# Performance work log

Measured on AMD Instinct MI355X. Metric: run time of the kernel, lower is better.

## Reference

```python
import jax, jax.numpy as jnp
import numpy as np

B, T, N, F = 16, 24, 2048, 64


def setup_inputs() -> dict:
    key = jax.random.key(0)
    kx, k1, k2, k3, kb, kv = jax.random.split(key, 6)
    x = jax.random.normal(kx, (B, T, N, F), dtype=jnp.float32)
    # xavier_uniform for U2 (N,F) and Ve (T,T); uniform(0,1) for U1, U3, be
    lim_u2 = float(np.sqrt(6.0 / (N + F)))
    lim_ve = float(np.sqrt(6.0 / (T + T)))
    U1 = jax.random.uniform(k1, (N,), dtype=jnp.float32)
    U2 = jax.random.uniform(k2, (N, F), dtype=jnp.float32, minval=-lim_u2, maxval=lim_u2)
    U3 = jax.random.uniform(k3, (F,), dtype=jnp.float32)
    be = jax.random.uniform(kb, (T, T), dtype=jnp.float32)
    Ve = jax.random.uniform(kv, (T, T), dtype=jnp.float32, minval=-lim_ve, maxval=lim_ve)
    return {"x": x, "U1": U1, "U2": U2, "U3": U3, "be": be, "Ve": Ve}


def reference(x, U1, U2, U3, be, Ve):
    # lhs: contract x over N with U1 -> (B,T,F), then project by U2^T -> (B,T,N)
    lhs = jnp.einsum('btnf,n->btf', x, U1) @ U2.T            # (B,T,N)
    # rhs: contract x over F with U3 -> (B,T,N)
    rhs = jnp.einsum('btnf,f->btn', x, U3)                   # (B,T,N)
    # temporal score matrix (B,T,T)
    product = jnp.einsum('btn,bsn->bts', lhs, rhs)
    E = jnp.einsum('ts,bsr->btr', Ve, jax.nn.sigmoid(product + be))
    A = jax.nn.softmax(E, axis=1)                            # softmax over dim=1 (t)
    # out[b,s,n,f] = sum_t x[b,t,n,f] * A[b,t,s]
    return jnp.einsum('btnf,bts->bsnf', x, A)
```

## Files before the change

### kernel.cpp

```cpp
#include <hip/hip_runtime.h>
#include <math.h>

#define BB 16
#define TT 24
#define NN 2048
#define FF 64
#define BT (BB*TT)
#define T2 (TT*TT)
#define NF4 (NN*FF/4)

#define WS_T1   0
#define WS_RHS  (WS_T1  + BT*FF)
#define WS_LHS  (WS_RHS + BT*NN)
#define WS_SIG  (WS_LHS + BT*NN)
#define WS_AMAT (WS_SIG + BB*T2)

__device__ __forceinline__ float4 f4zero() { return make_float4(0.f,0.f,0.f,0.f); }

__global__ __launch_bounds__(256) void k_stage1(
    const float4* __restrict__ x4, const float* __restrict__ U1,
    const float4* __restrict__ U3_4, float* __restrict__ t1,
    float* __restrict__ rhs)
{
    const int bt    = blockIdx.x;
    const int nbase = blockIdx.y * 512;
    const int tid   = threadIdx.x;
    const int wave  = tid >> 6;
    const int lane  = tid & 63;
    const int rowg  = lane >> 4;
    const int fq    = lane & 15;

    const float4 u3 = U3_4[fq];
    float4 t1a = f4zero();
    const float4* xb = x4 + (size_t)bt * NF4;

    for (int i = 0; i < 32; ++i) {
        const int n = nbase + i*16 + wave*4 + rowg;
        const float4 xv = xb[(size_t)n*16 + fq];
        const float u1n = U1[n];
        t1a.x += xv.x*u1n; t1a.y += xv.y*u1n; t1a.z += xv.z*u1n; t1a.w += xv.w*u1n;
        float r = xv.x*u3.x + xv.y*u3.y + xv.z*u3.z + xv.w*u3.w;
        r += __shfl_xor(r, 8);
        r += __shfl_xor(r, 4);
        r += __shfl_xor(r, 2);
        r += __shfl_xor(r, 1);
        if (fq == 0) rhs[(size_t)bt*NN + n] = r;
    }
    t1a.x += __shfl_xor(t1a.x, 16); t1a.y += __shfl_xor(t1a.y, 16);
    t1a.z += __shfl_xor(t1a.z, 16); t1a.w += __shfl_xor(t1a.w, 16);
    t1a.x += __shfl_xor(t1a.x, 32); t1a.y += __shfl_xor(t1a.y, 32);
    t1a.z += __shfl_xor(t1a.z, 32); t1a.w += __shfl_xor(t1a.w, 32);

    __shared__ float4 red[4][16];
    if (lane < 16) red[wave][lane] = t1a;
    __syncthreads();
    if (tid < 16) {
        const float4 s0 = red[0][tid], s1 = red[1][tid], s2 = red[2][tid], s3 = red[3][tid];
        float4 tot;
        tot.x = s0.x+s1.x+s2.x+s3.x; tot.y = s0.y+s1.y+s2.y+s3.y;
        tot.z = s0.z+s1.z+s2.z+s3.z; tot.w = s0.w+s1.w+s2.w+s3.w;
        float* dst = t1 + (size_t)bt*FF + tid*4;
        atomicAdd(dst+0, tot.x); atomicAdd(dst+1, tot.y);
        atomicAdd(dst+2, tot.z); atomicAdd(dst+3, tot.w);
    }
}

__global__ __launch_bounds__(256) void k_lhs(
    const float4* __restrict__ t1_4, const float4* __restrict__ U2_4,
    float* __restrict__ lhs)
{
    const int tid = threadIdx.x;
    const int n   = blockIdx.x*256 + tid;
    const int btb = blockIdx.y*32;

    __shared__ float4 t1s[32*16];
    t1s[tid]       = t1_4[(size_t)btb*16 + tid];
    t1s[tid + 256] = t1_4[(size_t)btb*16 + tid + 256];
    __syncthreads();

    float4 u2r[16];
    #pragma unroll
    for (int k = 0; k < 16; ++k) u2r[k] = U2_4[(size_t)n*16 + k];

    for (int bl = 0; bl < 32; ++bl) {
        float acc = 0.f;
        #pragma unroll
        for (int k = 0; k < 16; ++k) {
            const float4 tv = t1s[bl*16 + k];
            acc += u2r[k].x*tv.x + u2r[k].y*tv.y + u2r[k].z*tv.z + u2r[k].w*tv.w;
        }
        lhs[(size_t)(btb+bl)*NN + n] = acc;
    }
}

__global__ __launch_bounds__(256) void k_prod(
    const float4* __restrict__ lhs4, const float4* __restrict__ rhs4,
    const float* __restrict__ be, float* __restrict__ sig)
{
    const int tid  = threadIdx.x;
    const int wave = tid >> 6, lane = tid & 63;
    const int gw   = blockIdx.x*4 + wave;
    const int b    = gw / T2;
    const int rem  = gw % T2;
    const int i    = rem / TT;
    const int j    = rem % TT;

    const float4* L = lhs4 + (size_t)(b*TT + i)*(NN/4);
    const float4* R = rhs4 + (size_t)(b*TT + j)*(NN/4);
    float acc = 0.f;
    for (int k = lane; k < NN/4; k += 64) {
        const float4 l = L[k], r = R[k];
        acc += l.x*r.x + l.y*r.y + l.z*r.z + l.w*r.w;
    }
    #pragma unroll
    for (int m = 32; m >= 1; m >>= 1) acc += __shfl_xor(acc, m);
    if (lane == 0) {
        const float p = acc + be[i*TT + j];
        sig[(size_t)(b*TT + i)*TT + j] = 1.0f / (1.0f + expf(-p));
    }
}

__global__ __launch_bounds__(576) void k_softmax(
    const float* __restrict__ sig, const float* __restrict__ Ve,
    float* __restrict__ Amat)
{
    const int b = blockIdx.x, tid = threadIdx.x;
    __shared__ float sigL[T2], VeL[T2], EL[T2], eL[T2];
    sigL[tid] = sig[(size_t)b*T2 + tid];
    VeL[tid]  = Ve[tid];
    __syncthreads();

    const int t = tid / TT, r = tid % TT;
    float E = 0.f;
    #pragma unroll
    for (int s = 0; s < TT; ++s) E += VeL[t*TT + s] * sigL[s*TT + r];
    EL[tid] = E;
    __syncthreads();

    float m = -1e30f;
    for (int tt = 0; tt < TT; ++tt) m = fmaxf(m, EL[tt*TT + r]);
    const float e = expf(E - m);
    eL[tid] = e;
    __syncthreads();

    float ssum = 0.f;
    for (int tt = 0; tt < TT; ++tt) ssum += eL[tt*TT + r];
    Amat[(size_t)b*T2 + tid] = e / ssum;
}

__global__ __launch_bounds__(256) void k_out(
    const float4* __restrict__ x4, const float4* __restrict__ Amat4,
    float4* __restrict__ out4)
{
    const int b   = blockIdx.y;
    const int idx = blockIdx.x*256 + threadIdx.x;

    __shared__ float4 A4[TT*6];
    if (threadIdx.x < TT*6) A4[threadIdx.x] = Amat4[(size_t)b*TT*6 + threadIdx.x];
    __syncthreads();

    const float4* xb = x4 + (size_t)b*TT*NF4;
    float4 acc[TT];
    #pragma unroll
    for (int s = 0; s < TT; ++s) acc[s] = f4zero();

    for (int t = 0; t < TT; ++t) {
        const float4 xv = xb[(size_t)t*NF4 + idx];
        #pragma unroll
        for (int sq = 0; sq < 6; ++sq) {
            const float4 a = A4[t*6 + sq];
            acc[4*sq+0].x += xv.x*a.x; acc[4*sq+0].y += xv.y*a.x;
            acc[4*sq+0].z += xv.z*a.x; acc[4*sq+0].w += xv.w*a.x;
            acc[4*sq+1].x += xv.x*a.y; acc[4*sq+1].y += xv.y*a.y;
            acc[4*sq+1].z += xv.z*a.y; acc[4*sq+1].w += xv.w*a.y;
            acc[4*sq+2].x += xv.x*a.z; acc[4*sq+2].y += xv.y*a.z;
            acc[4*sq+2].z += xv.z*a.z; acc[4*sq+2].w += xv.w*a.z;
            acc[4*sq+3].x += xv.x*a.w; acc[4*sq+3].y += xv.y*a.w;
            acc[4*sq+3].z += xv.z*a.w; acc[4*sq+3].w += xv.w*a.w;
        }
    }
    float4* ob = out4 + (size_t)b*TT*NF4;
    #pragma unroll
    for (int s = 0; s < TT; ++s) ob[(size_t)s*NF4 + idx] = acc[s];
}

extern "C" void kernel_launch(void* const* d_in, const int* in_sizes, int n_in,
                              void* d_out, int out_size, void* d_ws, size_t ws_size,
                              hipStream_t stream)
{
    const float* x  = (const float*)d_in[0];
    const float* U1 = (const float*)d_in[1];
    const float* U2 = (const float*)d_in[2];
    const float* U3 = (const float*)d_in[3];
    const float* be = (const float*)d_in[4];
    const float* Ve = (const float*)d_in[5];

    float* ws  = (float*)d_ws;
    float* t1  = ws + WS_T1;
    float* rhs = ws + WS_RHS;
    float* lhs = ws + WS_LHS;
    float* sg  = ws + WS_SIG;
    float* Am  = ws + WS_AMAT;

    hipMemsetAsync(t1, 0, (size_t)BT*FF*sizeof(float), stream);

    k_stage1<<<dim3(BT, 4), 256, 0, stream>>>(
        (const float4*)x, U1, (const float4*)U3, t1, rhs);
    k_lhs<<<dim3(8, 12), 256, 0, stream>>>(
        (const float4*)t1, (const float4*)U2, lhs);
    k_prod<<<dim3((BB*T2)/4), 256, 0, stream>>>(
        (const float4*)lhs, (const float4*)rhs, be, sg);
    k_softmax<<<dim3(BB), 576, 0, stream>>>(sg, Ve, Am);
    k_out<<<dim3(NF4/256, BB), 256, 0, stream>>>(
        (const float4*)x, (const float4*)Am, (float4*)d_out);
}
```

Measured before the change: 412.2 us.

## Reassociate score matmul via U2 projection of rhs and fuse attention stages

Rewrites product = (t1·U2ᵀ)·rhsᵀ as t1·(U2ᵀ·rhs), so stage1 accumulates a 64-wide r2 = rhs·U2 per (b,t) instead of writing full N-length lhs/rhs arrays. The lhs projection and prod kernels are removed and the 24x24 score, sigmoid, Ve mix and softmax are fused into one per-batch kernel. Atomics and the memset are replaced by per-chunk partial sums that the attention kernel adds up. The output kernel also switches to nontemporal stores. This cuts launches and large workspace traffic, at the cost of extra U2 loads in stage1 and changed summation order.

New measurement: 380.1 us. 1.08x faster.

```diff
diff --git a/kernel.cpp b/kernel.cpp
--- a/kernel.cpp
+++ b/kernel.cpp
@@ -9,21 +9,28 @@
 #define T2 (TT*TT)
 #define NF4 (NN*FF/4)
 
-#define WS_T1   0
-#define WS_RHS  (WS_T1  + BT*FF)
-#define WS_LHS  (WS_RHS + BT*NN)
-#define WS_SIG  (WS_LHS + BT*NN)
-#define WS_AMAT (WS_SIG + BB*T2)
+#define WS_T1P  0
+#define WS_R2P  (WS_T1P + 4*BT*FF)
+#define WS_AMAT (WS_R2P + 4*BT*FF)
+
+typedef float vfloat4 __attribute__((ext_vector_type(4)));
 
 __device__ __forceinline__ float4 f4zero() { return make_float4(0.f,0.f,0.f,0.f); }
 
+__device__ __forceinline__ void nt_store_f4(float4 v, float4* p) {
+    vfloat4 nv;
+    nv.x = v.x; nv.y = v.y; nv.z = v.z; nv.w = v.w;
+    __builtin_nontemporal_store(nv, (vfloat4*)p);
+}
+
 __global__ __launch_bounds__(256) void k_stage1(
     const float4* __restrict__ x4, const float* __restrict__ U1,
-    const float4* __restrict__ U3_4, float* __restrict__ t1,
-    float* __restrict__ rhs)
+    const float4* __restrict__ U3_4, const float4* __restrict__ U2_4,
+    float4* __restrict__ t1p, float4* __restrict__ r2p)
 {
     const int bt    = blockIdx.x;
-    const int nbase = blockIdx.y * 512;
+    const int chunk = blockIdx.y;
+    const int nbase = chunk * 512;
     const int tid   = threadIdx.x;
     const int wave  = tid >> 6;
     const int lane  = tid & 63;
@@ -32,6 +39,7 @@
 
     const float4 u3 = U3_4[fq];
     float4 t1a = f4zero();
+    float4 r2a = f4zero();
     const float4* xb = x4 + (size_t)bt * NF4;
 
     for (int i = 0; i < 32; ++i) {
@@ -44,107 +52,84 @@
         r += __shfl_xor(r, 4);
         r += __shfl_xor(r, 2);
         r += __shfl_xor(r, 1);
-        if (fq == 0) rhs[(size_t)bt*NN + n] = r;
+        const float4 u2 = U2_4[(size_t)n*16 + fq];
+        r2a.x += r*u2.x; r2a.y += r*u2.y; r2a.z += r*u2.z; r2a.w += r*u2.w;
     }
     t1a.x += __shfl_xor(t1a.x, 16); t1a.y += __shfl_xor(t1a.y, 16);
     t1a.z += __shfl_xor(t1a.z, 16); t1a.w += __shfl_xor(t1a.w, 16);
     t1a.x += __shfl_xor(t1a.x, 32); t1a.y += __shfl_xor(t1a.y, 32);
     t1a.z += __shfl_xor(t1a.z, 32); t1a.w += __shfl_xor(t1a.w, 32);
+    r2a.x += __shfl_xor(r2a.x, 16); r2a.y += __shfl_xor(r2a.y, 16);
+    r2a.z += __shfl_xor(r2a.z, 16); r2a.w += __shfl_xor(r2a.w, 16);
+    r2a.x += __shfl_xor(r2a.x, 32); r2a.y += __shfl_xor(r2a.y, 32);
+    r2a.z += __shfl_xor(r2a.z, 32); r2a.w += __shfl_xor(r2a.w, 32);
 
-    __shared__ float4 red[4][16];
-    if (lane < 16) red[wave][lane] = t1a;
+    __shared__ float4 redT[4][16];
+    __shared__ float4 redR[4][16];
+    if (lane < 16) { redT[wave][lane] = t1a; redR[wave][lane] = r2a; }
     __syncthreads();
     if (tid < 16) {
-        const float4 s0 = red[0][tid], s1 = red[1][tid], s2 = red[2][tid], s3 = red[3][tid];
+        const float4 s0 = redT[0][tid], s1 = redT[1][tid], s2 = redT[2][tid], s3 = redT[3][tid];
         float4 tot;
         tot.x = s0.x+s1.x+s2.x+s3.x; tot.y = s0.y+s1.y+s2.y+s3.y;
         tot.z = s0.z+s1.z+s2.z+s3.z; tot.w = s0.w+s1.w+s2.w+s3.w;
-        float* dst = t1 + (size_t)bt*FF + tid*4;
-        atomicAdd(dst+0, tot.x); atomicAdd(dst+1, tot.y);
-        atomicAdd(dst+2, tot.z); atomicAdd(dst+3, tot.w);
+        t1p[((size_t)chunk*BT + bt)*16 + tid] = tot;
+    } else if (tid < 32) {
+        const int q = tid - 16;
+        const float4 s0 = redR[0][q], s1 = redR[1][q], s2 = redR[2][q], s3 = redR[3][q];
+        float4 tot;
+        tot.x = s0.x+s1.x+s2.x+s3.x; tot.y = s0.y+s1.y+s2.y+s3.y;
+        tot.z = s0.z+s1.z+s2.z+s3.z; tot.w = s0.w+s1.w+s2.w+s3.w;
+        r2p[((size_t)chunk*BT + bt)*16 + q] = tot;
     }
 }
 
-__global__ __launch_bounds__(256) void k_lhs(
-    const float4* __restrict__ t1_4, const float4* __restrict__ U2_4,
-    float* __restrict__ lhs)
-{
-    const int tid = threadIdx.x;
-    const int n   = blockIdx.x*256 + tid;
-    const int btb = blockIdx.y*32;
-
-    __shared__ float4 t1s[32*16];
-    t1s[tid]       = t1_4[(size_t)btb*16 + tid];
-    t1s[tid + 256] = t1_4[(size_t)btb*16 + tid + 256];
-    __syncthreads();
-
-    float4 u2r[16];
-    #pragma unroll
-    for (int k = 0; k < 16; ++k) u2r[k] = U2_4[(size_t)n*16 + k];
-
-    for (int bl = 0; bl < 32; ++bl) {
-        float acc = 0.f;
-        #pragma unroll
-        for (int k = 0; k < 16; ++k) {
-            const float4 tv = t1s[bl*16 + k];
-            acc += u2r[k].x*tv.x + u2r[k].y*tv.y + u2r[k].z*tv.z + u2r[k].w*tv.w;
-        }
-        lhs[(size_t)(btb+bl)*NN + n] = acc;
-    }
-}
-
-__global__ __launch_bounds__(256) void k_prod(
-    const float4* __restrict__ lhs4, const float4* __restrict__ rhs4,
-    const float* __restrict__ be, float* __restrict__ sig)
-{
-    const int tid  = threadIdx.x;
-    const int wave = tid >> 6, lane = tid & 63;
-    const int gw   = blockIdx.x*4 + wave;
-    const int b    = gw / T2;
-    const int rem  = gw % T2;
-    const int i    = rem / TT;
-    const int j    = rem % TT;
-
-    const float4* L = lhs4 + (size_t)(b*TT + i)*(NN/4);
-    const float4* R = rhs4 + (size_t)(b*TT + j)*(NN/4);
-    float acc = 0.f;
-    for (int k = lane; k < NN/4; k += 64) {
-        const float4 l = L[k], r = R[k];
-        acc += l.x*r.x + l.y*r.y + l.z*r.z + l.w*r.w;
-    }
-    #pragma unroll
-    for (int m = 32; m >= 1; m >>= 1) acc += __shfl_xor(acc, m);
-    if (lane == 0) {
-        const float p = acc + be[i*TT + j];
-        sig[(size_t)(b*TT + i)*TT + j] = 1.0f / (1.0f + expf(-p));
-    }
-}
-
-__global__ __launch_bounds__(576) void k_softmax(
-    const float* __restrict__ sig, const float* __restrict__ Ve,
+__global__ __launch_bounds__(576) void k_attn(
+    const float* __restrict__ t1p, const float* __restrict__ r2p,
+    const float* __restrict__ be, const float* __restrict__ Ve,
     float* __restrict__ Amat)
 {
     const int b = blockIdx.x, tid = threadIdx.x;
-    __shared__ float sigL[T2], VeL[T2], EL[T2], eL[T2];
-    sigL[tid] = sig[(size_t)b*T2 + tid];
-    VeL[tid]  = Ve[tid];
+    __shared__ float t1s[TT*FF];
+    __shared__ float r2s[TT*65];
+    __shared__ float VeL[T2];
+    __shared__ float sigL[TT*25];
+    __shared__ float EL[TT*25];
+    __shared__ float eL[TT*25];
+
+    for (int idx = tid; idx < TT*FF; idx += 576) {
+        const size_t base = (size_t)b*TT*FF + idx;
+        t1s[idx] = t1p[base] + t1p[base + BT*FF] + t1p[base + 2*BT*FF] + t1p[base + 3*BT*FF];
+        const float s2 = r2p[base] + r2p[base + BT*FF] + r2p[base + 2*BT*FF] + r2p[base + 3*BT*FF];
+        r2s[(idx >> 6)*65 + (idx & 63)] = s2;
+    }
+    VeL[tid] = Ve[tid];
     __syncthreads();
 
-    const int t = tid / TT, r = tid % TT;
+    const int i = tid / TT, j = tid % TT;
+    float p = 0.f;
+    #pragma unroll
+    for (int f = 0; f < FF; ++f) p += t1s[i*FF + f] * r2s[j*65 + f];
+    const float sg = 1.0f / (1.0f + expf(-(p + be[tid])));
+    sigL[i*25 + j] = sg;
+    __syncthreads();
+
     float E = 0.f;
     #pragma unroll
-    for (int s = 0; s < TT; ++s) E += VeL[t*TT + s] * sigL[s*TT + r];
-    EL[tid] = E;
+    for (int s = 0; s < TT; ++s) E += VeL[i*TT + s] * sigL[s*25 + j];
+    EL[i*25 + j] = E;
     __syncthreads();
 
     float m = -1e30f;
-    for (int tt = 0; tt < TT; ++tt) m = fmaxf(m, EL[tt*TT + r]);
+    #pragma unroll
+    for (int t = 0; t < TT; ++t) m = fmaxf(m, EL[t*25 + j]);
     const float e = expf(E - m);
-    eL[tid] = e;
+    eL[i*25 + j] = e;
     __syncthreads();
 
     float ssum = 0.f;
-    for (int tt = 0; tt < TT; ++tt) ssum += eL[tt*TT + r];
+    #pragma unroll
+    for (int t = 0; t < TT; ++t) ssum += eL[t*25 + j];
     Amat[(size_t)b*T2 + tid] = e / ssum;
 }
 
@@ -181,7 +166,8 @@
     }
     float4* ob = out4 + (size_t)b*TT*NF4;
     #pragma unroll
-    for (int s = 0; s < TT; ++s) ob[(size_t)s*NF4 + idx] = acc[s];
+    for (int s = 0; s < TT; ++s)
+        nt_store_f4(acc[s], &ob[(size_t)s*NF4 + idx]);
 }
 
 extern "C" void kernel_launch(void* const* d_in, const int* in_sizes, int n_in,
@@ -195,22 +181,15 @@
     const float* be = (const float*)d_in[4];
     const float* Ve = (const float*)d_in[5];
 
-    float* ws  = (float*)d_ws;
-    float* t1  = ws + WS_T1;
-    float* rhs = ws + WS_RHS;
-    float* lhs = ws + WS_LHS;
-    float* sg  = ws + WS_SIG;
-    float* Am  = ws + WS_AMAT;
-
-    hipMemsetAsync(t1, 0, (size_t)BT*FF*sizeof(float), stream);
+    float* ws   = (float*)d_ws;
+    float* t1p  = ws + WS_T1P;
+    float* r2p  = ws + WS_R2P;
+    float* Am   = ws + WS_AMAT;
 
     k_stage1<<<dim3(BT, 4), 256, 0, stream>>>(
-        (const float4*)x, U1, (const float4*)U3, t1, rhs);
-    k_lhs<<<dim3(8, 12), 256, 0, stream>>>(
-        (const float4*)t1, (const float4*)U2, lhs);
-    k_prod<<<dim3((BB*T2)/4), 256, 0, stream>>>(
-        (const float4*)lhs, (const float4*)rhs, be, sg);
-    k_softmax<<<dim3(BB), 576, 0, stream>>>(sg, Ve, Am);
+        (const float4*)x, U1, (const float4*)U3, (const float4*)U2,
+        (float4*)t1p, (float4*)r2p);
+    k_attn<<<dim3(BB), 576, 0, stream>>>(t1p, r2p, be, Ve, Am);
     k_out<<<dim3(NF4/256, BB), 256, 0, stream>>>(
         (const float4*)x, (const float4*)Am, (float4*)d_out);
 }
```
